# Optimization experiments

Measured on AMD Instinct MI355X. Metric: run time of the kernel, lower is better.

## Reference

```python
import jax, jax.numpy as jnp
import numpy as np

HID = 128
OUT = 1
L = 4
N_NODES = 50000
N_EDGES = 600000
NUM_GRAPHS = 256
ATOM_FEATS, ATOM_VOCAB = 9, 64
BOND_FEATS, BOND_VOCAB = 3, 8
BN_EPS = 1e-5


def setup_inputs() -> dict:
    key = jax.random.key(0)
    ks = jax.random.split(key, 16)
    x = jax.random.randint(ks[0], (N_NODES, ATOM_FEATS), 0, ATOM_VOCAB)
    edge_index = jax.random.randint(ks[1], (2, N_EDGES), 0, N_NODES)
    edge_attr = jax.random.randint(ks[2], (N_EDGES, BOND_FEATS), 0, BOND_VOCAB)
    batch = jnp.sort(jax.random.randint(ks[3], (N_NODES,), 0, NUM_GRAPHS))
    s = 0.05
    atom_emb = jax.random.normal(ks[4], (ATOM_FEATS, ATOM_VOCAB, HID), jnp.float32) * s
    bond_emb = jax.random.normal(ks[5], (BOND_FEATS, BOND_VOCAB, HID), jnp.float32) * s
    lin1_w = jax.random.normal(ks[6], (L, HID, HID), jnp.float32) * (1.0 / np.sqrt(HID))
    lin1_b = jnp.zeros((L, HID), jnp.float32)
    lin2_w = jax.random.normal(ks[7], (L, HID, HID), jnp.float32) * (1.0 / np.sqrt(HID))
    lin2_b = jnp.zeros((L, HID), jnp.float32)
    bn_gamma = jnp.ones((L, HID), jnp.float32)
    bn_beta = jnp.zeros((L, HID), jnp.float32)
    bn_mean = jax.random.normal(ks[8], (L, HID), jnp.float32) * 0.1
    bn_var = jax.random.uniform(ks[9], (L, HID), jnp.float32, 0.5, 1.5)
    mlp_w = jax.random.normal(ks[10], (HID, OUT), jnp.float32) * (1.0 / np.sqrt(HID))
    mlp_b = jnp.zeros((OUT,), jnp.float32)
    return dict(x=x, edge_index=edge_index, edge_attr=edge_attr, batch=batch,
                atom_emb=atom_emb, bond_emb=bond_emb,
                lin1_w=lin1_w, lin1_b=lin1_b, lin2_w=lin2_w, lin2_b=lin2_b,
                bn_gamma=bn_gamma, bn_beta=bn_beta, bn_mean=bn_mean, bn_var=bn_var,
                mlp_w=mlp_w, mlp_b=mlp_b)


def _multi_embed(tables, idx):
    # tables: [F, V, H], idx: [N, F] -> sum over F of tables[f][idx[:, f]] -> [N, H]
    return jax.vmap(lambda tab, i: tab[i], in_axes=(0, 1))(tables, idx).sum(0)


def reference(x, edge_index, edge_attr, batch, atom_emb, bond_emb,
              lin1_w, lin1_b, lin2_w, lin2_b, bn_gamma, bn_beta,
              bn_mean, bn_var, mlp_w, mlp_b):
    h = _multi_embed(atom_emb, x)            # [N, H]
    e = _multi_embed(bond_emb, edge_attr)    # [E, H]
    src, dst = edge_index[0], edge_index[1]
    for l in range(L):
        x_res = h
        # GINEConv (eps=0): MLP(x + sum_j ReLU(x_j + e_ji))
        msg = jax.nn.relu(h[src] + e)                          # [E, H]
        agg = jax.ops.segment_sum(msg, dst, num_segments=N_NODES)
        z = h + agg
        z = jax.nn.relu(z @ lin1_w[l] + lin1_b[l]) @ lin2_w[l] + lin2_b[l]
        # BatchNorm (eval: running stats)
        z = (z - bn_mean[l]) * (bn_gamma[l] / jnp.sqrt(bn_var[l] + BN_EPS)) + bn_beta[l]
        h = x_res + jax.nn.relu(z)
        # dropout is identity in eval mode
    sums = jax.ops.segment_sum(h, batch, num_segments=NUM_GRAPHS)
    cnt = jax.ops.segment_sum(jnp.ones((N_NODES, 1), h.dtype), batch, num_segments=NUM_GRAPHS)
    pooled = sums / jnp.maximum(cnt, 1.0)
    return pooled @ mlp_w + mlp_b
```

## Files before the change

### kernel.cpp

```cpp
#include <hip/hip_runtime.h>

#define NNODES 50000
#define NEDGES 600000
#define NGRAPH 256
#define HD     128
#define NLAYER 4
#define NBLK_SCAN 49
#define NDEG 8

typedef __bf16 bf16;
typedef __attribute__((ext_vector_type(2))) __bf16 bf16x2;
typedef __attribute__((ext_vector_type(8))) __bf16 bf16x8;
typedef __attribute__((ext_vector_type(4))) float  f32x4;

#define CB_MLPW 0
#define CB_MLPB 128

#define PB_W    128
#define PB_BN   (PB_W + 2)
#define PB_MLP  (PB_BN + 1)
#define PB_ETAB (PB_MLP + 64)
#define PB_EMB  (PB_ETAB + 12500)
#define PB_HIST (PB_EMB + 293)

struct PtrPack { const void* p[12]; };

__device__ __forceinline__ float ldf(const void* p, int i, int flag) {
    return flag ? (float)((const bf16*)p)[i] : ((const float*)p)[i];
}
__device__ __forceinline__ float blo(unsigned u) { return __uint_as_float(u << 16); }
__device__ __forceinline__ float bhi(unsigned u) { return __uint_as_float(u & 0xFFFF0000u); }

__global__ __launch_bounds__(256) void k_prep(PtrPack pk, const int* __restrict__ x,
                                              const int* __restrict__ ei,
                                              float* __restrict__ cvt, bf16* __restrict__ wtg,
                                              float* __restrict__ biasf, float* __restrict__ scalef,
                                              float* __restrict__ shiftf, bf16* __restrict__ etab,
                                              bf16* __restrict__ hbuf, int* __restrict__ deg8) {
    const int flag = (((const unsigned*)pk.p[6])[0] != 0x3F800000u);
    int b = blockIdx.x, t = threadIdx.x;
    if (b < PB_W) {
#pragma unroll
        for (int it = 0; it < 4; ++it) {
            int idx = (b << 10) + (it << 8) + t;
            int mat = idx >> 14, rem = idx & 16383;
            int k = rem & 127, n = rem >> 7;
            const void* src = (mat < 4) ? pk.p[2] : pk.p[4];
            int mi = (mat < 4) ? mat : mat - 4;
            wtg[((size_t)mat << 14) + (n << 7) + k] = (bf16)ldf(src, (mi << 14) + (k << 7) + n, flag);
        }
    } else if (b < PB_BN) {
        int i = (b - PB_W) * 256 + t;
        biasf[i] = ldf(pk.p[3], i, flag);
        float s = ldf(pk.p[6], i, flag) * rsqrtf(ldf(pk.p[9], i, flag) + 1e-5f);
        scalef[i] = s;
        shiftf[i] = (ldf(pk.p[5], i, flag) - ldf(pk.p[8], i, flag)) * s + ldf(pk.p[7], i, flag);
    } else if (b < PB_MLP) {
        if (t < 128)       cvt[CB_MLPW + t] = ldf(pk.p[10], t, flag);
        else if (t == 128) cvt[CB_MLPB] = ldf(pk.p[11], 0, flag);
    } else if (b < PB_ETAB) {
#pragma unroll
        for (int it = 0; it < 4; ++it) {
            int idx = ((b - PB_MLP) << 10) + (it << 8) + t;
            int combo = idx >> 7, ch = idx & 127;
            int c0 = combo & 7, c1 = (combo >> 3) & 7, c2 = combo >> 6;
            float v = ldf(pk.p[1], (c0 << 7) + ch, flag) +
                      ldf(pk.p[1], ((8 + c1) << 7) + ch, flag) +
                      ldf(pk.p[1], ((16 + c2) << 7) + ch, flag);
            etab[idx] = (bf16)v;
        }
    } else if (b < PB_EMB) {
        int wid = t >> 6, lane = t & 63;
        int n = (b - PB_ETAB) * 4 + wid;
        if (n >= NNODES) return;
        const int* xr = x + n * 9;
        float ax = 0.f, ay = 0.f;
        if (flag) {
            const char* ae = (const char*)pk.p[0];
#pragma unroll
            for (int f = 0; f < 9; ++f) {
                int v = xr[f];
                unsigned hu = *(const unsigned*)(ae + (((size_t)(f * 64 + v)) << 8) + (lane << 2));
                ax += blo(hu); ay += bhi(hu);
            }
        } else {
            const float* ae = (const float*)pk.p[0];
#pragma unroll
            for (int f = 0; f < 9; ++f) {
                int v = xr[f];
                float2 tv = ((const float2*)(ae + (((size_t)(f * 64 + v)) << 7)))[lane];
                ax += tv.x; ay += tv.y;
            }
        }
        bf16x2 hv; hv[0] = (bf16)ax; hv[1] = (bf16)ay;
        ((bf16x2*)(hbuf + ((size_t)n << 7)))[lane] = hv;
    } else {
        int i0 = (b - PB_EMB) * 2048 + t;
#pragma unroll
        for (int k = 0; k < 8; ++k) {
            int i = i0 + k * 256;
            if (i < NEDGES) atomicAdd(&deg8[(b & (NDEG - 1)) * NNODES + ei[NEDGES + i]], 1);
        }
    }
}

__global__ void k_scan1(const int* __restrict__ deg8, int* __restrict__ partials) {
    __shared__ int s[256];
    int t = threadIdx.x, b = blockIdx.x;
    int base = b * 1024 + t * 4;
    int sum = 0;
#pragma unroll
    for (int i = 0; i < 4; ++i) {
        int idx = base + i;
        if (idx < NNODES)
#pragma unroll
            for (int c = 0; c < NDEG; ++c) sum += deg8[c * NNODES + idx];
    }
    s[t] = sum; __syncthreads();
    for (int o = 128; o > 0; o >>= 1) { if (t < o) s[t] += s[t + o]; __syncthreads(); }
    if (t == 0) partials[b] = s[0];
}

__global__ void k_scan3(const int* __restrict__ deg8, const int* __restrict__ partials,
                        int* __restrict__ row_start, int* __restrict__ cursor) {
    __shared__ int s[256];
    __shared__ int boff;
    int t = threadIdx.x, b = blockIdx.x;
    if (t < 64) {
        int own = (t < b && t < NBLK_SCAN) ? partials[t] : 0;
#pragma unroll
        for (int o = 32; o > 0; o >>= 1) own += __shfl_xor(own, o);
        if (t == 0) boff = own;
    }
    int base = b * 1024 + t * 4;
    int v[4]; int sum = 0;
#pragma unroll
    for (int i = 0; i < 4; ++i) {
        int idx = base + i;
        int d = 0;
        if (idx < NNODES)
#pragma unroll
            for (int c = 0; c < NDEG; ++c) d += deg8[c * NNODES + idx];
        v[i] = d;
        sum += d;
    }
    s[t] = sum; __syncthreads();
    for (int o = 1; o < 256; o <<= 1) {
        int add = (t >= o) ? s[t - o] : 0;
        __syncthreads();
        s[t] += add;
        __syncthreads();
    }
    int run = s[t] - sum + boff;
#pragma unroll
    for (int i = 0; i < 4; ++i) {
        int idx = base + i;
        if (idx < NNODES) { row_start[idx] = run; cursor[idx] = run; }
        run += v[i];
    }
    if (b == NBLK_SCAN - 1 && t == 255) row_start[NNODES] = run;
}

__global__ void k_fill(const int* __restrict__ ei, const int* __restrict__ ea,
                       int* __restrict__ cursor, unsigned* __restrict__ payload) {
    int i = blockIdx.x * 256 + threadIdx.x;
    if (i >= NEDGES) return;
    int dst = ei[NEDGES + i];
    int pos = atomicAdd(&cursor[dst], 1);
    unsigned p = (unsigned)ei[i] | ((unsigned)ea[3 * i] << 16) |
                 ((unsigned)ea[3 * i + 1] << 19) | ((unsigned)ea[3 * i + 2] << 22);
    payload[pos] = p;
}

__global__ __launch_bounds__(256) void k_agg(const bf16* __restrict__ hbuf,
                                             const bf16* __restrict__ etab,
                                             const int* __restrict__ row_start,
                                             const unsigned* __restrict__ payload,
                                             bf16* __restrict__ zbuf) {
    const int t = threadIdx.x;
    const int wid = t >> 6, lane = t & 63;
    const int quad = lane >> 4, l16 = lane & 15;
    const int n = blockIdx.x * 4 + wid;
    if (n >= NNODES) return;
    const int beg = row_start[n], end = row_start[n + 1];
    const char* hbp = (const char*)hbuf;
    const char* ebp = (const char*)etab;

    uint4 hn = {0u, 0u, 0u, 0u};
    if (quad == 0) hn = *(const uint4*)(hbp + ((size_t)n << 8) + (l16 << 4));

    float acc[8];
#pragma unroll
    for (int k = 0; k < 8; ++k) acc[k] = 0.f;

    for (int base = beg; base < end; base += 16) {
        int m = end - base; if (m > 16) m = 16;
        unsigned pe[4]; uint4 he[4]; uint4 ee[4];
#pragma unroll
        for (int i = 0; i < 4; ++i) {
            int ii = (i << 2) + quad;
            pe[i] = payload[base + (ii < m ? ii : 0)];
        }
#pragma unroll
        for (int i = 0; i < 4; ++i) {
            he[i] = *(const uint4*)(hbp + (((size_t)(pe[i] & 0xFFFFu)) << 8) + (l16 << 4));
            ee[i] = *(const uint4*)(ebp + (((size_t)((pe[i] >> 16) & 511u)) << 8) + (l16 << 4));
        }
#pragma unroll
        for (int i = 0; i < 4; ++i) {
            bool ok = ((i << 2) + quad) < m;
            float m0 = fmaxf(blo(he[i].x) + blo(ee[i].x), 0.f);
            float m1 = fmaxf(bhi(he[i].x) + bhi(ee[i].x), 0.f);
            float m2 = fmaxf(blo(he[i].y) + blo(ee[i].y), 0.f);
            float m3 = fmaxf(bhi(he[i].y) + bhi(ee[i].y), 0.f);
            float m4 = fmaxf(blo(he[i].z) + blo(ee[i].z), 0.f);
            float m5 = fmaxf(bhi(he[i].z) + bhi(ee[i].z), 0.f);
            float m6 = fmaxf(blo(he[i].w) + blo(ee[i].w), 0.f);
            float m7 = fmaxf(bhi(he[i].w) + bhi(ee[i].w), 0.f);
            if (ok) {
                acc[0] += m0; acc[1] += m1; acc[2] += m2; acc[3] += m3;
                acc[4] += m4; acc[5] += m5; acc[6] += m6; acc[7] += m7;
            }
        }
    }

#pragma unroll
    for (int k = 0; k < 8; ++k) {
        acc[k] += __shfl_xor(acc[k], 16);
        acc[k] += __shfl_xor(acc[k], 32);
    }
    if (quad == 0) {
        bf16x8 z;
        z[0] = (bf16)(blo(hn.x) + acc[0]); z[1] = (bf16)(bhi(hn.x) + acc[1]);
        z[2] = (bf16)(blo(hn.y) + acc[2]); z[3] = (bf16)(bhi(hn.y) + acc[3]);
        z[4] = (bf16)(blo(hn.z) + acc[4]); z[5] = (bf16)(bhi(hn.z) + acc[5]);
        z[6] = (bf16)(blo(hn.w) + acc[6]); z[7] = (bf16)(bhi(hn.w) + acc[7]);
        *(bf16x8*)(zbuf + ((size_t)n << 7) + (l16 << 3)) = z;
    }
}

__global__ __launch_bounds__(256) void k_update(const bf16* __restrict__ zbuf,
                                                bf16* __restrict__ hbuf,
                                                const bf16* __restrict__ wtg,
                                                const float* __restrict__ biasf,
                                                const float* __restrict__ scalef,
                                                const float* __restrict__ shiftf,
                                                int layer) {
    __shared__ __align__(16) bf16 zs[64 * 128];
    __shared__ __align__(16) bf16 wt[128 * 128];
    const int t = threadIdx.x;
    const int w = t >> 6, lane = t & 63, r16 = lane & 15, q = lane >> 4;
    const int m0 = blockIdx.x * 64;

#pragma unroll
    for (int it = 0; it < 4; ++it) {
        int idx = t + it * 256;
        int r = idx >> 4, c = idx & 15;
        int row = m0 + r;
        bf16x8 v;
        if (row < NNODES) v = *(const bf16x8*)(zbuf + ((size_t)row << 7) + (c << 3));
        else { for (int ii = 0; ii < 8; ++ii) v[ii] = (bf16)0.0f; }
        *(bf16x8*)&zs[(r << 7) + ((c ^ (r & 7)) << 3)] = v;
    }
    {
        const bf16* w1 = wtg + ((size_t)layer << 14);
#pragma unroll
        for (int it = 0; it < 8; ++it) {
            int idx = t + it * 256;
            int r = idx >> 4, c = idx & 15;
            *(bf16x8*)&wt[(r << 7) + ((c ^ (r & 7)) << 3)] =
                *(const bf16x8*)(w1 + (r << 7) + (c << 3));
        }
    }
    bf16x8 w2r[8];
    {
        const bf16* w2 = wtg + ((size_t)(NLAYER + layer) << 14);
#pragma unroll
        for (int it = 0; it < 8; ++it) {
            int idx = t + it * 256;
            int r = idx >> 4, c = idx & 15;
            w2r[it] = *(const bf16x8*)(w2 + (r << 7) + (c << 3));
        }
    }
    __syncthreads();

    f32x4 acc[8];
#pragma unroll
    for (int j = 0; j < 8; ++j) acc[j] = (f32x4){0.f, 0.f, 0.f, 0.f};

    const int sw = r16 & 7;
#pragma unroll
    for (int kc = 0; kc < 4; ++kc) {
        int col = (((kc << 2) + q) ^ sw) << 3;
        bf16x8 a0 = *(const bf16x8*)&zs[((w * 16 + r16) << 7) + col];
        bf16x8 bb[8];
#pragma unroll
        for (int j = 0; j < 8; ++j) bb[j] = *(const bf16x8*)&wt[((j * 16 + r16) << 7) + col];
#pragma unroll
        for (int j = 0; j < 8; ++j)
            acc[j] = __builtin_amdgcn_mfma_f32_16x16x32_bf16(a0, bb[j], acc[j], 0, 0, 0);
    }
    {
        const float* b1 = biasf + (layer << 7);
#pragma unroll
        for (int j = 0; j < 8; ++j) {
            int n = j * 16 + r16;
            float bi = b1[n];
#pragma unroll
            for (int rg = 0; rg < 4; ++rg) {
                int row = w * 16 + q * 4 + rg;
                float v = fmaxf(acc[j][rg] + bi, 0.f);
                zs[(row << 7) + (((n >> 3) ^ (row & 7)) << 3) + (n & 7)] = (bf16)v;
            }
        }
    }
    __syncthreads();
#pragma unroll
    for (int it = 0; it < 8; ++it) {
        int idx = t + it * 256;
        int r = idx >> 4, c = idx & 15;
        *(bf16x8*)&wt[(r << 7) + ((c ^ (r & 7)) << 3)] = w2r[it];
    }
    __syncthreads();

#pragma unroll
    for (int j = 0; j < 8; ++j) acc[j] = (f32x4){0.f, 0.f, 0.f, 0.f};

#pragma unroll
    for (int kc = 0; kc < 4; ++kc) {
        int col = (((kc << 2) + q) ^ sw) << 3;
        bf16x8 a0 = *(const bf16x8*)&zs[((w * 16 + r16) << 7) + col];
        bf16x8 bb[8];
#pragma unroll
        for (int j = 0; j < 8; ++j) bb[j] = *(const bf16x8*)&wt[((j * 16 + r16) << 7) + col];
#pragma unroll
        for (int j = 0; j < 8; ++j)
            acc[j] = __builtin_amdgcn_mfma_f32_16x16x32_bf16(a0, bb[j], acc[j], 0, 0, 0);
    }
    {
        const float* sc = scalef + (layer << 7);
        const float* sh = shiftf + (layer << 7);
#pragma unroll
        for (int j = 0; j < 8; ++j) {
            int n = j * 16 + r16;
            float s_ = sc[n], h_ = sh[n];
#pragma unroll
            for (int rg = 0; rg < 4; ++rg) {
                int row = w * 16 + q * 4 + rg;
                float z = acc[j][rg] * s_ + h_;
                zs[(row << 7) + (((n >> 3) ^ (row & 7)) << 3) + (n & 7)] = (bf16)fmaxf(z, 0.f);
            }
        }
    }
    __syncthreads();
#pragma unroll
    for (int it = 0; it < 4; ++it) {
        int c = t + it * 256;
        int row = c >> 4, seg = c & 15;
        int grow = m0 + row;
        if (grow < NNODES) {
            bf16x8 zv = *(const bf16x8*)&zs[(row << 7) + ((seg ^ (row & 7)) << 3)];
            bf16* hp = hbuf + ((size_t)grow << 7) + (seg << 3);
            bf16x8 hv = *(const bf16x8*)hp;
            bf16x8 r;
#pragma unroll
            for (int k = 0; k < 8; ++k) r[k] = (bf16)((float)hv[k] + (float)zv[k]);
            *(bf16x8*)hp = r;
        }
    }
}

__global__ __launch_bounds__(256) void k_pool(const bf16* __restrict__ hbuf,
                                              const int* __restrict__ batch,
                                              const float* __restrict__ cvt,
                                              const unsigned* __restrict__ gam_raw,
                                              void* __restrict__ out) {
    const int flag = (*gam_raw != 0x3F800000u);
    int g = blockIdx.x;
    int t = threadIdx.x, wid = t >> 6, lane = t & 63;
    int lo = 0, hi = NNODES;
    while (lo < hi) { int m = (lo + hi) >> 1; if (batch[m] < g) lo = m + 1; else hi = m; }
    int s = lo;
    hi = NNODES;
    while (lo < hi) { int m = (lo + hi) >> 1; if (batch[m] <= g) lo = m + 1; else hi = m; }
    int e = lo;
    float ax = 0.f, ay = 0.f;
    for (int n = s + wid; n < e; n += 4) {
        unsigned hu = ((const unsigned*)(hbuf + ((size_t)n << 7)))[lane];
        ax += blo(hu);
        ay += bhi(hu);
    }
    __shared__ float red[4][128];
    red[wid][2 * lane] = ax;
    red[wid][2 * lane + 1] = ay;
    __syncthreads();
    __shared__ float fin[128];
    if (t < 128) {
        float sum = red[0][t] + red[1][t] + red[2][t] + red[3][t];
        float cnt = fmaxf((float)(e - s), 1.0f);
        fin[t] = (sum / cnt) * cvt[CB_MLPW + t];
    }
    __syncthreads();
    for (int o = 64; o > 0; o >>= 1) {
        if (t < o) fin[t] += fin[t + o];
        __syncthreads();
    }
    if (t == 0) {
        float r = fin[0] + cvt[CB_MLPB];
        if (flag) ((bf16*)out)[g] = (bf16)r;
        else      ((float*)out)[g] = r;
    }
}

extern "C" void kernel_launch(void* const* d_in, const int* in_sizes, int n_in,
                              void* d_out, int out_size, void* d_ws, size_t ws_size,
                              hipStream_t stream) {
    const int* x     = (const int*)d_in[0];
    const int* ei    = (const int*)d_in[1];
    const int* ea    = (const int*)d_in[2];
    const int* batch = (const int*)d_in[3];

    char* ws = (char*)d_ws;
    size_t o = 0;
    auto alloc = [&](size_t bytes) -> void* {
        void* p = ws + o;
        o = (o + bytes + 255) & ~(size_t)255;
        return p;
    };
    bf16*     hbuf      = (bf16*)alloc((size_t)NNODES * HD * 2);
    bf16*     zbuf      = (bf16*)alloc((size_t)NNODES * HD * 2);
    unsigned* payload   = (unsigned*)alloc((size_t)NEDGES * 4);
    int*      row_start = (int*)alloc((size_t)(NNODES + 1) * 4);
    int*      cursor    = (int*)alloc((size_t)NNODES * 4);
    int*      deg8      = (int*)alloc((size_t)NDEG * NNODES * 4);
    int*      partials  = (int*)alloc(64 * 4);
    bf16*     wtg       = (bf16*)alloc((size_t)8 * 128 * 128 * 2);
    bf16*     etab      = (bf16*)alloc((size_t)512 * 128 * 2);
    float*    cvt       = (float*)alloc((size_t)129 * 4);
    float*    biasf     = (float*)alloc(NLAYER * HD * 4);
    float*    scalef    = (float*)alloc(NLAYER * HD * 4);
    float*    shiftf    = (float*)alloc(NLAYER * HD * 4);

    PtrPack pk;
    for (int i = 0; i < 12; ++i) pk.p[i] = d_in[4 + i];
    const unsigned* gam_raw = (const unsigned*)d_in[10];

    hipMemsetAsync(deg8, 0, (size_t)NDEG * NNODES * 4, stream);
    k_prep<<<PB_HIST, 256, 0, stream>>>(pk, x, ei, cvt, wtg, biasf, scalef, shiftf, etab, hbuf, deg8);
    k_scan1<<<NBLK_SCAN, 256, 0, stream>>>(deg8, partials);
    k_scan3<<<NBLK_SCAN, 256, 0, stream>>>(deg8, partials, row_start, cursor);
    k_fill<<<(NEDGES + 255) / 256, 256, 0, stream>>>(ei, ea, cursor, payload);
    for (int l = 0; l < NLAYER; ++l) {
        k_agg<<<(NNODES + 3) / 4, 256, 0, stream>>>(hbuf, etab, row_start, payload, zbuf);
        k_update<<<(NNODES + 63) / 64, 256, 0, stream>>>(zbuf, hbuf, wtg, biasf, scalef, shiftf, l);
    }
    k_pool<<<NGRAPH, 256, 0, stream>>>(hbuf, batch, cvt, gam_raw, d_out);
}
```

Measured before the change: 380.1 us.

## Switch activations to fp16 with packed-half math in edge aggregation

Replaces bf16 storage and MFMA with fp16 throughout, so the edge-aggregation kernel can add and ReLU messages with packed half-precision vector ops instead of unpacking each value to fp32. Partial sums are kept in fp16 for up to four edges per lane before being added into fp32 accumulators. The edge payload is now read once per 32 edges with a coalesced load and handed to lanes by shuffle, and the self-feature load moves to the epilogue. The weight-transpose loop is reordered so the reads are coalesced. The cost is fp16's narrower range and the extra rounding from partial sums kept in half precision.

New measurement: 364.1 us. 4.2% less time.

```diff
diff --git a/kernel.cpp b/kernel.cpp
--- a/kernel.cpp
+++ b/kernel.cpp
@@ -9,8 +9,9 @@
 #define NDEG 8
 
 typedef __bf16 bf16;
-typedef __attribute__((ext_vector_type(2))) __bf16 bf16x2;
-typedef __attribute__((ext_vector_type(8))) __bf16 bf16x8;
+typedef _Float16 f16;
+typedef __attribute__((ext_vector_type(2))) _Float16 f16x2;
+typedef __attribute__((ext_vector_type(8))) _Float16 f16x8;
 typedef __attribute__((ext_vector_type(4))) float  f32x4;
 
 #define CB_MLPW 0
@@ -33,10 +34,10 @@
 
 __global__ __launch_bounds__(256) void k_prep(PtrPack pk, const int* __restrict__ x,
                                               const int* __restrict__ ei,
-                                              float* __restrict__ cvt, bf16* __restrict__ wtg,
+                                              float* __restrict__ cvt, f16* __restrict__ wtg,
                                               float* __restrict__ biasf, float* __restrict__ scalef,
-                                              float* __restrict__ shiftf, bf16* __restrict__ etab,
-                                              bf16* __restrict__ hbuf, int* __restrict__ deg8) {
+                                              float* __restrict__ shiftf, f16* __restrict__ etab,
+                                              f16* __restrict__ hbuf, int* __restrict__ deg8) {
     const int flag = (((const unsigned*)pk.p[6])[0] != 0x3F800000u);
     int b = blockIdx.x, t = threadIdx.x;
     if (b < PB_W) {
@@ -44,10 +45,10 @@
         for (int it = 0; it < 4; ++it) {
             int idx = (b << 10) + (it << 8) + t;
             int mat = idx >> 14, rem = idx & 16383;
-            int k = rem & 127, n = rem >> 7;
+            int n = rem & 127, k = rem >> 7;
             const void* src = (mat < 4) ? pk.p[2] : pk.p[4];
             int mi = (mat < 4) ? mat : mat - 4;
-            wtg[((size_t)mat << 14) + (n << 7) + k] = (bf16)ldf(src, (mi << 14) + (k << 7) + n, flag);
+            wtg[((size_t)mat << 14) + (n << 7) + k] = (f16)ldf(src, (mi << 14) + (k << 7) + n, flag);
         }
     } else if (b < PB_BN) {
         int i = (b - PB_W) * 256 + t;
@@ -67,7 +68,7 @@
             float v = ldf(pk.p[1], (c0 << 7) + ch, flag) +
                       ldf(pk.p[1], ((8 + c1) << 7) + ch, flag) +
                       ldf(pk.p[1], ((16 + c2) << 7) + ch, flag);
-            etab[idx] = (bf16)v;
+            etab[idx] = (f16)v;
         }
     } else if (b < PB_EMB) {
         int wid = t >> 6, lane = t & 63;
@@ -92,8 +93,8 @@
                 ax += tv.x; ay += tv.y;
             }
         }
-        bf16x2 hv; hv[0] = (bf16)ax; hv[1] = (bf16)ay;
-        ((bf16x2*)(hbuf + ((size_t)n << 7)))[lane] = hv;
+        f16x2 hv; hv[0] = (f16)ax; hv[1] = (f16)ay;
+        ((f16x2*)(hbuf + ((size_t)n << 7)))[lane] = hv;
     } else {
         int i0 = (b - PB_EMB) * 2048 + t;
 #pragma unroll
@@ -172,11 +173,11 @@
     payload[pos] = p;
 }
 
-__global__ __launch_bounds__(256) void k_agg(const bf16* __restrict__ hbuf,
-                                             const bf16* __restrict__ etab,
+__global__ __launch_bounds__(256) void k_agg(const f16* __restrict__ hbuf,
+                                             const f16* __restrict__ etab,
                                              const int* __restrict__ row_start,
                                              const unsigned* __restrict__ payload,
-                                             bf16* __restrict__ zbuf) {
+                                             f16* __restrict__ zbuf) {
     const int t = threadIdx.x;
     const int wid = t >> 6, lane = t & 63;
     const int quad = lane >> 4, l16 = lane & 15;
@@ -186,41 +187,45 @@
     const char* hbp = (const char*)hbuf;
     const char* ebp = (const char*)etab;
 
-    uint4 hn = {0u, 0u, 0u, 0u};
-    if (quad == 0) hn = *(const uint4*)(hbp + ((size_t)n << 8) + (l16 << 4));
-
+    const f16x2 z2 = {0, 0};
     float acc[8];
 #pragma unroll
     for (int k = 0; k < 8; ++k) acc[k] = 0.f;
 
-    for (int base = beg; base < end; base += 16) {
-        int m = end - base; if (m > 16) m = 16;
-        unsigned pe[4]; uint4 he[4]; uint4 ee[4];
-#pragma unroll
-        for (int i = 0; i < 4; ++i) {
-            int ii = (i << 2) + quad;
-            pe[i] = payload[base + (ii < m ? ii : 0)];
-        }
-#pragma unroll
-        for (int i = 0; i < 4; ++i) {
-            he[i] = *(const uint4*)(hbp + (((size_t)(pe[i] & 0xFFFFu)) << 8) + (l16 << 4));
-            ee[i] = *(const uint4*)(ebp + (((size_t)((pe[i] >> 16) & 511u)) << 8) + (l16 << 4));
-        }
-#pragma unroll
-        for (int i = 0; i < 4; ++i) {
-            bool ok = ((i << 2) + quad) < m;
-            float m0 = fmaxf(blo(he[i].x) + blo(ee[i].x), 0.f);
-            float m1 = fmaxf(bhi(he[i].x) + bhi(ee[i].x), 0.f);
-            float m2 = fmaxf(blo(he[i].y) + blo(ee[i].y), 0.f);
-            float m3 = fmaxf(bhi(he[i].y) + bhi(ee[i].y), 0.f);
-            float m4 = fmaxf(blo(he[i].z) + blo(ee[i].z), 0.f);
-            float m5 = fmaxf(bhi(he[i].z) + bhi(ee[i].z), 0.f);
-            float m6 = fmaxf(blo(he[i].w) + blo(ee[i].w), 0.f);
-            float m7 = fmaxf(bhi(he[i].w) + bhi(ee[i].w), 0.f);
-            if (ok) {
-                acc[0] += m0; acc[1] += m1; acc[2] += m2; acc[3] += m3;
-                acc[4] += m4; acc[5] += m5; acc[6] += m6; acc[7] += m7;
-            }
+    for (int base = beg; base < end; base += 32) {
+        int m = end - base; if (m > 32) m = 32;
+        unsigned pv = (base + lane < end) ? payload[base + lane] : 0u;
+        for (int j = 0; j < m; j += 16) {
+            unsigned pe[4]; f16x8 he[4]; f16x8 ee[4];
+#pragma unroll
+            for (int i = 0; i < 4; ++i) {
+                int idx = j + i * 4 + quad;
+                pe[i] = __shfl(pv, idx < m ? idx : 0);
+            }
+#pragma unroll
+            for (int i = 0; i < 4; ++i) {
+                he[i] = *(const f16x8*)(hbp + (((size_t)(pe[i] & 0xFFFFu)) << 8) + (l16 << 4));
+                ee[i] = *(const f16x8*)(ebp + (((size_t)((pe[i] >> 16) & 511u)) << 8) + (l16 << 4));
+            }
+            f16x2 ca[4] = {z2, z2, z2, z2};
+#pragma unroll
+            for (int i = 0; i < 4; ++i) {
+                bool ok = (j + i * 4 + quad) < m;
+                if (ok) {
+                    f16x2 s0 = (f16x2){he[i][0], he[i][1]} + (f16x2){ee[i][0], ee[i][1]};
+                    f16x2 s1 = (f16x2){he[i][2], he[i][3]} + (f16x2){ee[i][2], ee[i][3]};
+                    f16x2 s2 = (f16x2){he[i][4], he[i][5]} + (f16x2){ee[i][4], ee[i][5]};
+                    f16x2 s3 = (f16x2){he[i][6], he[i][7]} + (f16x2){ee[i][6], ee[i][7]};
+                    ca[0] += __builtin_elementwise_max(s0, z2);
+                    ca[1] += __builtin_elementwise_max(s1, z2);
+                    ca[2] += __builtin_elementwise_max(s2, z2);
+                    ca[3] += __builtin_elementwise_max(s3, z2);
+                }
+            }
+            acc[0] += (float)ca[0][0]; acc[1] += (float)ca[0][1];
+            acc[2] += (float)ca[1][0]; acc[3] += (float)ca[1][1];
+            acc[4] += (float)ca[2][0]; acc[5] += (float)ca[2][1];
+            acc[6] += (float)ca[3][0]; acc[7] += (float)ca[3][1];
         }
     }
 
@@ -230,24 +235,23 @@
         acc[k] += __shfl_xor(acc[k], 32);
     }
     if (quad == 0) {
-        bf16x8 z;
-        z[0] = (bf16)(blo(hn.x) + acc[0]); z[1] = (bf16)(bhi(hn.x) + acc[1]);
-        z[2] = (bf16)(blo(hn.y) + acc[2]); z[3] = (bf16)(bhi(hn.y) + acc[3]);
-        z[4] = (bf16)(blo(hn.z) + acc[4]); z[5] = (bf16)(bhi(hn.z) + acc[5]);
-        z[6] = (bf16)(blo(hn.w) + acc[6]); z[7] = (bf16)(bhi(hn.w) + acc[7]);
-        *(bf16x8*)(zbuf + ((size_t)n << 7) + (l16 << 3)) = z;
-    }
-}
-
-__global__ __launch_bounds__(256) void k_update(const bf16* __restrict__ zbuf,
-                                                bf16* __restrict__ hbuf,
-                                                const bf16* __restrict__ wtg,
+        f16x8 hn = *(const f16x8*)(hbp + ((size_t)n << 8) + (l16 << 4));
+        f16x8 z;
+#pragma unroll
+        for (int k = 0; k < 8; ++k) z[k] = (f16)((float)hn[k] + acc[k]);
+        *(f16x8*)(zbuf + ((size_t)n << 7) + (l16 << 3)) = z;
+    }
+}
+
+__global__ __launch_bounds__(256) void k_update(const f16* __restrict__ zbuf,
+                                                f16* __restrict__ hbuf,
+                                                const f16* __restrict__ wtg,
                                                 const float* __restrict__ biasf,
                                                 const float* __restrict__ scalef,
                                                 const float* __restrict__ shiftf,
                                                 int layer) {
-    __shared__ __align__(16) bf16 zs[64 * 128];
-    __shared__ __align__(16) bf16 wt[128 * 128];
+    __shared__ __align__(16) f16 zs[64 * 128];
+    __shared__ __align__(16) f16 wt[128 * 128];
     const int t = threadIdx.x;
     const int w = t >> 6, lane = t & 63, r16 = lane & 15, q = lane >> 4;
     const int m0 = blockIdx.x * 64;
@@ -257,29 +261,29 @@
         int idx = t + it * 256;
         int r = idx >> 4, c = idx & 15;
         int row = m0 + r;
-        bf16x8 v;
-        if (row < NNODES) v = *(const bf16x8*)(zbuf + ((size_t)row << 7) + (c << 3));
-        else { for (int ii = 0; ii < 8; ++ii) v[ii] = (bf16)0.0f; }
-        *(bf16x8*)&zs[(r << 7) + ((c ^ (r & 7)) << 3)] = v;
+        f16x8 v;
+        if (row < NNODES) v = *(const f16x8*)(zbuf + ((size_t)row << 7) + (c << 3));
+        else { for (int ii = 0; ii < 8; ++ii) v[ii] = (f16)0.0f; }
+        *(f16x8*)&zs[(r << 7) + ((c ^ (r & 7)) << 3)] = v;
     }
     {
-        const bf16* w1 = wtg + ((size_t)layer << 14);
+        const f16* w1 = wtg + ((size_t)layer << 14);
 #pragma unroll
         for (int it = 0; it < 8; ++it) {
             int idx = t + it * 256;
             int r = idx >> 4, c = idx & 15;
-            *(bf16x8*)&wt[(r << 7) + ((c ^ (r & 7)) << 3)] =
-                *(const bf16x8*)(w1 + (r << 7) + (c << 3));
-        }
-    }
-    bf16x8 w2r[8];
+            *(f16x8*)&wt[(r << 7) + ((c ^ (r & 7)) << 3)] =
+                *(const f16x8*)(w1 + (r << 7) + (c << 3));
+        }
+    }
+    f16x8 w2r[8];
     {
-        const bf16* w2 = wtg + ((size_t)(NLAYER + layer) << 14);
+        const f16* w2 = wtg + ((size_t)(NLAYER + layer) << 14);
 #pragma unroll
         for (int it = 0; it < 8; ++it) {
             int idx = t + it * 256;
             int r = idx >> 4, c = idx & 15;
-            w2r[it] = *(const bf16x8*)(w2 + (r << 7) + (c << 3));
+            w2r[it] = *(const f16x8*)(w2 + (r << 7) + (c << 3));
         }
     }
     __syncthreads();
@@ -292,13 +296,13 @@
 #pragma unroll
     for (int kc = 0; kc < 4; ++kc) {
         int col = (((kc << 2) + q) ^ sw) << 3;
-        bf16x8 a0 = *(const bf16x8*)&zs[((w * 16 + r16) << 7) + col];
-        bf16x8 bb[8];
-#pragma unroll
-        for (int j = 0; j < 8; ++j) bb[j] = *(const bf16x8*)&wt[((j * 16 + r16) << 7) + col];
+        f16x8 a0 = *(const f16x8*)&zs[((w * 16 + r16) << 7) + col];
+        f16x8 bb[8];
+#pragma unroll
+        for (int j = 0; j < 8; ++j) bb[j] = *(const f16x8*)&wt[((j * 16 + r16) << 7) + col];
 #pragma unroll
         for (int j = 0; j < 8; ++j)
-            acc[j] = __builtin_amdgcn_mfma_f32_16x16x32_bf16(a0, bb[j], acc[j], 0, 0, 0);
+            acc[j] = __builtin_amdgcn_mfma_f32_16x16x32_f16(a0, bb[j], acc[j], 0, 0, 0);
     }
     {
         const float* b1 = biasf + (layer << 7);
@@ -310,7 +314,7 @@
             for (int rg = 0; rg < 4; ++rg) {
                 int row = w * 16 + q * 4 + rg;
                 float v = fmaxf(acc[j][rg] + bi, 0.f);
-                zs[(row << 7) + (((n >> 3) ^ (row & 7)) << 3) + (n & 7)] = (bf16)v;
+                zs[(row << 7) + (((n >> 3) ^ (row & 7)) << 3) + (n & 7)] = (f16)v;
             }
         }
     }
@@ -319,7 +323,7 @@
     for (int it = 0; it < 8; ++it) {
         int idx = t + it * 256;
         int r = idx >> 4, c = idx & 15;
-        *(bf16x8*)&wt[(r << 7) + ((c ^ (r & 7)) << 3)] = w2r[it];
+        *(f16x8*)&wt[(r << 7) + ((c ^ (r & 7)) << 3)] = w2r[it];
     }
     __syncthreads();
 
@@ -329,13 +333,13 @@
 #pragma unroll
     for (int kc = 0; kc < 4; ++kc) {
         int col = (((kc << 2) + q) ^ sw) << 3;
-        bf16x8 a0 = *(const bf16x8*)&zs[((w * 16 + r16) << 7) + col];
-        bf16x8 bb[8];
-#pragma unroll
-        for (int j = 0; j < 8; ++j) bb[j] = *(const bf16x8*)&wt[((j * 16 + r16) << 7) + col];
+        f16x8 a0 = *(const f16x8*)&zs[((w * 16 + r16) << 7) + col];
+        f16x8 bb[8];
+#pragma unroll
+        for (int j = 0; j < 8; ++j) bb[j] = *(const f16x8*)&wt[((j * 16 + r16) << 7) + col];
 #pragma unroll
         for (int j = 0; j < 8; ++j)
-            acc[j] = __builtin_amdgcn_mfma_f32_16x16x32_bf16(a0, bb[j], acc[j], 0, 0, 0);
+            acc[j] = __builtin_amdgcn_mfma_f32_16x16x32_f16(a0, bb[j], acc[j], 0, 0, 0);
     }
     {
         const float* sc = scalef + (layer << 7);
@@ -348,7 +352,7 @@
             for (int rg = 0; rg < 4; ++rg) {
                 int row = w * 16 + q * 4 + rg;
                 float z = acc[j][rg] * s_ + h_;
-                zs[(row << 7) + (((n >> 3) ^ (row & 7)) << 3) + (n & 7)] = (bf16)fmaxf(z, 0.f);
+                zs[(row << 7) + (((n >> 3) ^ (row & 7)) << 3) + (n & 7)] = (f16)fmaxf(z, 0.f);
             }
         }
     }
@@ -359,18 +363,18 @@
         int row = c >> 4, seg = c & 15;
         int grow = m0 + row;
         if (grow < NNODES) {
-            bf16x8 zv = *(const bf16x8*)&zs[(row << 7) + ((seg ^ (row & 7)) << 3)];
-            bf16* hp = hbuf + ((size_t)grow << 7) + (seg << 3);
-            bf16x8 hv = *(const bf16x8*)hp;
-            bf16x8 r;
-#pragma unroll
-            for (int k = 0; k < 8; ++k) r[k] = (bf16)((float)hv[k] + (float)zv[k]);
-            *(bf16x8*)hp = r;
-        }
-    }
-}
-
-__global__ __launch_bounds__(256) void k_pool(const bf16* __restrict__ hbuf,
+            f16x8 zv = *(const f16x8*)&zs[(row << 7) + ((seg ^ (row & 7)) << 3)];
+            f16* hp = hbuf + ((size_t)grow << 7) + (seg << 3);
+            f16x8 hv = *(const f16x8*)hp;
+            f16x8 r;
+#pragma unroll
+            for (int k = 0; k < 8; ++k) r[k] = (f16)((float)hv[k] + (float)zv[k]);
+            *(f16x8*)hp = r;
+        }
+    }
+}
+
+__global__ __launch_bounds__(256) void k_pool(const f16* __restrict__ hbuf,
                                               const int* __restrict__ batch,
                                               const float* __restrict__ cvt,
                                               const unsigned* __restrict__ gam_raw,
@@ -386,9 +390,9 @@
     int e = lo;
     float ax = 0.f, ay = 0.f;
     for (int n = s + wid; n < e; n += 4) {
-        unsigned hu = ((const unsigned*)(hbuf + ((size_t)n << 7)))[lane];
-        ax += blo(hu);
-        ay += bhi(hu);
+        f16x2 hu = ((const f16x2*)(hbuf + ((size_t)n << 7)))[lane];
+        ax += (float)hu[0];
+        ay += (float)hu[1];
     }
     __shared__ float red[4][128];
     red[wid][2 * lane] = ax;
@@ -427,15 +431,15 @@
         o = (o + bytes + 255) & ~(size_t)255;
         return p;
     };
-    bf16*     hbuf      = (bf16*)alloc((size_t)NNODES * HD * 2);
-    bf16*     zbuf      = (bf16*)alloc((size_t)NNODES * HD * 2);
+    f16*      hbuf      = (f16*)alloc((size_t)NNODES * HD * 2);
+    f16*      zbuf      = (f16*)alloc((size_t)NNODES * HD * 2);
     unsigned* payload   = (unsigned*)alloc((size_t)NEDGES * 4);
     int*      row_start = (int*)alloc((size_t)(NNODES + 1) * 4);
     int*      cursor    = (int*)alloc((size_t)NNODES * 4);
     int*      deg8      = (int*)alloc((size_t)NDEG * NNODES * 4);
     int*      partials  = (int*)alloc(64 * 4);
-    bf16*     wtg       = (bf16*)alloc((size_t)8 * 128 * 128 * 2);
-    bf16*     etab      = (bf16*)alloc((size_t)512 * 128 * 2);
+    f16*      wtg       = (f16*)alloc((size_t)8 * 128 * 128 * 2);
+    f16*      etab      = (f16*)alloc((size_t)512 * 128 * 2);
     float*    cvt       = (float*)alloc((size_t)129 * 4);
     float*    biasf     = (float*)alloc(NLAYER * HD * 4);
     float*    scalef    = (float*)alloc(NLAYER * HD * 4);
```
